# Optimization experiments

Hardware: AMD Instinct MI355X
Metric: run time of the kernel (lower is better)

Reference implementation:

```python
import jax, jax.numpy as jnp
import numpy as np

N, E = 10000, 320000
F_IN, HID, C_OUT = 256, 512, 128

def setup_inputs() -> dict:
    key = jax.random.key(0)
    ks = jax.random.split(key, 8)
    x = jax.random.normal(ks[0], (N, F_IN), dtype=jnp.float32)
    edge_index = jax.random.randint(ks[1], (2, E), 0, N, dtype=jnp.int64)
    s1 = 1.0 / np.sqrt(F_IN)
    s2 = 1.0 / np.sqrt(HID)
    # PyG SAGEConv: out = lin_l(aggr_sum(x_j)) + lin_r(x_i); lin_l has bias, lin_r does not
    W1l = jax.random.uniform(ks[2], (F_IN, HID), jnp.float32, -s1, s1)
    b1 = jnp.zeros((HID,), jnp.float32)
    W1r = jax.random.uniform(ks[3], (F_IN, HID), jnp.float32, -s1, s1)
    W2l = jax.random.uniform(ks[4], (HID, C_OUT), jnp.float32, -s2, s2)
    b2 = jnp.zeros((C_OUT,), jnp.float32)
    W2r = jax.random.uniform(ks[5], (HID, C_OUT), jnp.float32, -s2, s2)
    return {"x": x, "edge_index": edge_index, "W1l": W1l, "b1": b1,
            "W1r": W1r, "W2l": W2l, "b2": b2, "W2r": W2r}

def sage_conv(x, src, dst, Wl, b, Wr):
    # gather source-node features along edges, sum into target nodes, then linear
    agg = jax.ops.segment_sum(x[src], dst, num_segments=N)  # [N, F]
    return agg @ Wl + b + x @ Wr

def reference(x, edge_index, W1l, b1, W1r, W2l, b2, W2r):
    src, dst = edge_index[0], edge_index[1]
    h = sage_conv(x, src, dst, W1l, b1, W1r)
    h = jax.nn.relu(h)
    # F.dropout with training=False is identity (eval mode reference)
    out = sage_conv(h, src, dst, W2l, b2, W2r)
    return out
```

## Files before the change

### kernel.cpp

```cpp
#include <hip/hip_runtime.h>

#define N_NODES 10000
#define F_IN 256
#define HID 512
#define C_OUT 128
#define NEDGE 320000
#define BUCKET 128

typedef __attribute__((ext_vector_type(8))) short short8;
typedef __attribute__((ext_vector_type(4))) float floatx4;

__device__ inline float bf2f_lo(unsigned u) { union { float f; unsigned i; } v; v.i = u << 16; return v.f; }
__device__ inline float bf2f_hi(unsigned u) { union { float f; unsigned i; } v; v.i = u & 0xFFFF0000u; return v.f; }
__device__ inline unsigned short f2bf(float f) {
    union { float f; unsigned i; } v; v.f = f;
    unsigned r = (v.i + 0x7FFFu + ((v.i >> 16) & 1u)) >> 16;
    return (unsigned short)r;
}
__device__ inline void add8(float* a, uint4 v) {
    a[0] += bf2f_lo(v.x); a[1] += bf2f_hi(v.x);
    a[2] += bf2f_lo(v.y); a[3] += bf2f_hi(v.y);
    a[4] += bf2f_lo(v.z); a[5] += bf2f_hi(v.z);
    a[6] += bf2f_lo(v.w); a[7] += bf2f_hi(v.w);
}

__global__ __launch_bounds__(256)
void prep_kernel(const float4* __restrict__ xin, uint2* __restrict__ xb,
                 const float* __restrict__ W1l, const float* __restrict__ W1r,
                 const float* __restrict__ W2l, const float* __restrict__ W2r,
                 unsigned short* __restrict__ W1T, unsigned short* __restrict__ W2T,
                 int4* __restrict__ cursor4) {
    const int b = blockIdx.x;
    const int tid = threadIdx.x;
    if (b < 2500) {
        int i = b * 256 + tid;
        float4 v = xin[i];
        uint2 o;
        o.x = (unsigned)f2bf(v.x) | ((unsigned)f2bf(v.y) << 16);
        o.y = (unsigned)f2bf(v.z) | ((unsigned)f2bf(v.w) << 16);
        xb[i] = o;
        return;
    }
    if (b < 2884) {
        __shared__ float T[32][33];
        const int r = tid >> 3;
        const int c4 = (tid & 7) * 4;
        if (b < 2756) {
            int t = b - 2500;
            int kt = (t & 15) * 32, nt = (t >> 4) * 32;
            int kg = kt + r;
            const float* srcp = (kg < 256) ? (W1l + kg * 512) : (W1r + (kg - 256) * 512);
            float4 v = *(const float4*)(srcp + nt + c4);
            T[c4 + 0][r] = v.x; T[c4 + 1][r] = v.y; T[c4 + 2][r] = v.z; T[c4 + 3][r] = v.w;
            __syncthreads();
            ushort4 o;
            o.x = f2bf(T[r][c4 + 0]); o.y = f2bf(T[r][c4 + 1]);
            o.z = f2bf(T[r][c4 + 2]); o.w = f2bf(T[r][c4 + 3]);
            *(ushort4*)(W1T + (long long)(nt + r) * 512 + kt + c4) = o;
        } else {
            int t = b - 2756;
            int kt = (t & 15) * 32, col0 = (t >> 4) * 32;
            const float* Wsrc; int coloff;
            if (col0 < 128) { Wsrc = W2l; coloff = col0; } else { Wsrc = W2r; coloff = col0 - 128; }
            float4 v = *(const float4*)(Wsrc + (long long)(kt + r) * 128 + coloff + c4);
            T[c4 + 0][r] = v.x; T[c4 + 1][r] = v.y; T[c4 + 2][r] = v.z; T[c4 + 3][r] = v.w;
            __syncthreads();
            ushort4 o;
            o.x = f2bf(T[r][c4 + 0]); o.y = f2bf(T[r][c4 + 1]);
            o.z = f2bf(T[r][c4 + 2]); o.w = f2bf(T[r][c4 + 3]);
            *(ushort4*)(W2T + (long long)(col0 + r) * 512 + kt + c4) = o;
        }
        return;
    }
    {
        int i = (b - 2884) * 256 + tid;
        if (i < (N_NODES + 3) / 4) cursor4[i] = make_int4(0, 0, 0, 0);
    }
}

__global__ __launch_bounds__(256)
void fill_kernel(const int* __restrict__ src, const int* __restrict__ dst,
                 int* __restrict__ cursor, int* __restrict__ bucket, int E) {
    int e = blockIdx.x * 256 + threadIdx.x;
    if (e < E) {
        int d = dst[e];
        int pos = atomicAdd(&cursor[d], 1);
        bucket[(d << 7) + pos] = src[e];
    }
}

__global__ __launch_bounds__(256)
void gather_agg_256(const unsigned short* __restrict__ feat,
                    const int* __restrict__ cursor,
                    const int* __restrict__ bucket,
                    unsigned short* __restrict__ outp, int nnodes) {
    const int wid = (blockIdx.x * 256 + threadIdx.x) >> 6;
    if (wid >= nnodes) return;
    const int lane = threadIdx.x & 63;
    const int half = lane >> 5;
    const int sub = lane & 31;
    const long long myoff = (long long)sub * 8;
    const int cnt = __builtin_amdgcn_readfirstlane(cursor[wid]);
    const int* row = bucket + (wid << 7);

    float acc[8] = {0.f, 0.f, 0.f, 0.f, 0.f, 0.f, 0.f, 0.f};
    float accB[8] = {0.f, 0.f, 0.f, 0.f, 0.f, 0.f, 0.f, 0.f};

    int j = 0;
    for (; j + 8 <= cnt; j += 8) {
        const int4 ia = *(const int4*)(row + j);
        const int4 ib = *(const int4*)(row + j + 4);
        int i0 = half ? ia.y : ia.x;
        int i1 = half ? ia.w : ia.z;
        int i2 = half ? ib.y : ib.x;
        int i3 = half ? ib.w : ib.z;
        uint4 v0 = *(const uint4*)(feat + (long long)i0 * 256 + myoff);
        uint4 v1 = *(const uint4*)(feat + (long long)i1 * 256 + myoff);
        uint4 v2 = *(const uint4*)(feat + (long long)i2 * 256 + myoff);
        uint4 v3 = *(const uint4*)(feat + (long long)i3 * 256 + myoff);
        add8(acc, v0); add8(accB, v1); add8(acc, v2); add8(accB, v3);
    }
    for (; j + 2 <= cnt; j += 2) {
        const int2 e = *(const int2*)(row + j);
        int i0 = half ? e.y : e.x;
        uint4 v = *(const uint4*)(feat + (long long)i0 * 256 + myoff);
        add8(acc, v);
    }
    if (j < cnt) {
        int i0 = row[j];
        uint4 v = *(const uint4*)(feat + (long long)i0 * 256 + myoff);
        if (half == 0) add8(acc, v);
    }
#pragma unroll
    for (int k = 0; k < 8; ++k) acc[k] += accB[k];
#pragma unroll
    for (int k = 0; k < 8; ++k) acc[k] += __shfl_xor(acc[k], 32, 64);

    if (half == 0) {
        uint4 o;
        o.x = (unsigned)f2bf(acc[0]) | ((unsigned)f2bf(acc[1]) << 16);
        o.y = (unsigned)f2bf(acc[2]) | ((unsigned)f2bf(acc[3]) << 16);
        o.z = (unsigned)f2bf(acc[4]) | ((unsigned)f2bf(acc[5]) << 16);
        o.w = (unsigned)f2bf(acc[6]) | ((unsigned)f2bf(acc[7]) << 16);
        *(uint4*)(outp + (long long)wid * 256 + myoff) = o;
    }
}

__global__ __launch_bounds__(256)
void gather_acc_128(const unsigned short* __restrict__ feat,
                    const int* __restrict__ cursor,
                    const int* __restrict__ bucket,
                    float* __restrict__ outp, int nnodes) {
    const int wid = (blockIdx.x * 256 + threadIdx.x) >> 6;
    if (wid >= nnodes) return;
    const int lane = threadIdx.x & 63;
    const int g = lane >> 4;
    const int sub = lane & 15;
    const long long myoff = (long long)sub * 8;
    const int cnt = __builtin_amdgcn_readfirstlane(cursor[wid]);
    const int* row = bucket + (wid << 7);

    float4 c0 = make_float4(0.f, 0.f, 0.f, 0.f), c1 = c0;
    float* orow = outp + (long long)wid * 128 + sub * 8;
    if (lane < 16) {
        c0 = *(const float4*)(orow);
        c1 = *(const float4*)(orow + 4);
    }

    float acc[8] = {0.f, 0.f, 0.f, 0.f, 0.f, 0.f, 0.f, 0.f};
    float accB[8] = {0.f, 0.f, 0.f, 0.f, 0.f, 0.f, 0.f, 0.f};

    int j = 0;
    for (; j + 8 <= cnt; j += 8) {
        const int4 ia = *(const int4*)(row + j);
        const int4 ib = *(const int4*)(row + j + 4);
        int i0 = (g < 2) ? (g == 0 ? ia.x : ia.y) : (g == 2 ? ia.z : ia.w);
        int i1 = (g < 2) ? (g == 0 ? ib.x : ib.y) : (g == 2 ? ib.z : ib.w);
        uint4 v0 = *(const uint4*)(feat + (long long)i0 * 128 + myoff);
        uint4 v1 = *(const uint4*)(feat + (long long)i1 * 128 + myoff);
        add8(acc, v0); add8(accB, v1);
    }
    for (; j + 4 <= cnt; j += 4) {
        const int4 ia = *(const int4*)(row + j);
        int i0 = (g < 2) ? (g == 0 ? ia.x : ia.y) : (g == 2 ? ia.z : ia.w);
        uint4 v = *(const uint4*)(feat + (long long)i0 * 128 + myoff);
        add8(acc, v);
    }
    int rem = cnt - j;
    if (rem > 0) {
        int idx = row[j + (g < rem ? g : 0)];
        uint4 v = *(const uint4*)(feat + (long long)idx * 128 + myoff);
        if (g < rem) add8(acc, v);
    }
#pragma unroll
    for (int k = 0; k < 8; ++k) acc[k] += accB[k];
#pragma unroll
    for (int k = 0; k < 8; ++k) acc[k] += __shfl_xor(acc[k], 16, 64);
#pragma unroll
    for (int k = 0; k < 8; ++k) acc[k] += __shfl_xor(acc[k], 32, 64);

    if (lane < 16) {
        c0.x += acc[0]; c0.y += acc[1]; c0.z += acc[2]; c0.w += acc[3];
        c1.x += acc[4]; c1.y += acc[5]; c1.z += acc[6]; c1.w += acc[7];
        *(float4*)(orow) = c0;
        *(float4*)(orow + 4) = c1;
    }
}

template <int MODE>
__global__ __launch_bounds__(256)
void mfma_gemm(const unsigned short* __restrict__ A1, int K1,
               const unsigned short* __restrict__ A2, int K2,
               const unsigned short* __restrict__ BT,
               const float* __restrict__ bias,
               void* __restrict__ C0v, void* __restrict__ C1v,
               int M, int Nfull) {
    __shared__ unsigned short A_lds[64][72];
    __shared__ unsigned short B_lds[64][72];

    const int t = threadIdx.x;
    const int lane = t & 63;
    const int w = t >> 6;
    const int wm = w >> 1, wn = w & 1;
    const int l15 = lane & 15;
    const int quad = lane >> 4;
    const int row0 = blockIdx.x * 64;
    const int col0 = blockIdx.y * 64;
    const int Ktot = K1 + K2;

    floatx4 acc00 = {0.f, 0.f, 0.f, 0.f}, acc01 = acc00, acc10 = acc00, acc11 = acc00;

    for (int k0 = 0; k0 < Ktot; k0 += 64) {
        const unsigned short* Ap;
        int astride, acol;
        if (k0 < K1) { Ap = A1; astride = K1; acol = k0; }
        else         { Ap = A2; astride = K2; acol = k0 - K1; }
#pragma unroll
        for (int it = 0; it < 2; ++it) {
            int ch = t + it * 256;
            int row = ch >> 3, c16 = ch & 7;
            int gr = row0 + row; if (gr >= M) gr = M - 1;
            int4 av = *(const int4*)(Ap + (long long)gr * astride + acol + c16 * 8);
            *(int4*)&A_lds[row][c16 * 8] = av;
            int4 bv = *(const int4*)(BT + (long long)(col0 + row) * Ktot + k0 + c16 * 8);
            *(int4*)&B_lds[row][c16 * 8] = bv;
        }
        __syncthreads();
#pragma unroll
        for (int kc = 0; kc < 2; ++kc) {
            short8 a0 = *(short8*)&A_lds[wm * 32 + l15][kc * 32 + quad * 8];
            short8 a1 = *(short8*)&A_lds[wm * 32 + 16 + l15][kc * 32 + quad * 8];
            short8 b0 = *(short8*)&B_lds[wn * 32 + l15][kc * 32 + quad * 8];
            short8 b1 = *(short8*)&B_lds[wn * 32 + 16 + l15][kc * 32 + quad * 8];
            acc00 = __builtin_amdgcn_mfma_f32_16x16x32_bf16(a0, b0, acc00, 0, 0, 0);
            acc01 = __builtin_amdgcn_mfma_f32_16x16x32_bf16(a0, b1, acc01, 0, 0, 0);
            acc10 = __builtin_amdgcn_mfma_f32_16x16x32_bf16(a1, b0, acc10, 0, 0, 0);
            acc11 = __builtin_amdgcn_mfma_f32_16x16x32_bf16(a1, b1, acc11, 0, 0, 0);
        }
        __syncthreads();
    }

    const int cj0 = col0 + wn * 32 + l15;
    const int cj1 = cj0 + 16;
    const int rbase = row0 + wm * 32 + quad * 4;

    if (MODE == 0) {
        unsigned short* C0 = (unsigned short*)C0v;
        const float bi0 = bias[cj0], bi1 = bias[cj1];
        const floatx4* accs[2][2] = {{&acc00, &acc01}, {&acc10, &acc11}};
#pragma unroll
        for (int i = 0; i < 2; ++i) {
#pragma unroll
            for (int reg = 0; reg < 4; ++reg) {
                int r = rbase + i * 16 + reg;
                if (r >= M) continue;
                float v0 = fmaxf((*accs[i][0])[reg] + bi0, 0.f);
                float v1 = fmaxf((*accs[i][1])[reg] + bi1, 0.f);
                C0[(long long)r * Nfull + cj0] = f2bf(v0);
                C0[(long long)r * Nfull + cj1] = f2bf(v1);
            }
        }
    } else {
        const floatx4* accs[2][2] = {{&acc00, &acc01}, {&acc10, &acc11}};
        if (cj0 < 128) {
            unsigned short* C0 = (unsigned short*)C0v;
#pragma unroll
            for (int i = 0; i < 2; ++i) {
#pragma unroll
                for (int reg = 0; reg < 4; ++reg) {
                    int r = rbase + i * 16 + reg;
                    if (r >= M) continue;
                    C0[(long long)r * 128 + cj0] = f2bf((*accs[i][0])[reg]);
                    C0[(long long)r * 128 + cj1] = f2bf((*accs[i][1])[reg]);
                }
            }
        } else {
            float* C1 = (float*)C1v;
            const int d0 = cj0 - 128, d1 = cj1 - 128;
            const float bi0 = bias[d0], bi1 = bias[d1];
#pragma unroll
            for (int i = 0; i < 2; ++i) {
#pragma unroll
                for (int reg = 0; reg < 4; ++reg) {
                    int r = rbase + i * 16 + reg;
                    if (r >= M) continue;
                    C1[(long long)r * 128 + d0] = (*accs[i][0])[reg] + bi0;
                    C1[(long long)r * 128 + d1] = (*accs[i][1])[reg] + bi1;
                }
            }
        }
    }
}

extern "C" void kernel_launch(void* const* d_in, const int* in_sizes, int n_in,
                              void* d_out, int out_size, void* d_ws, size_t ws_size,
                              hipStream_t stream) {
    const float* x   = (const float*)d_in[0];
    const int*   ei  = (const int*)d_in[1];
    const float* W1l = (const float*)d_in[2];
    const float* b1  = (const float*)d_in[3];
    const float* W1r = (const float*)d_in[4];
    const float* W2l = (const float*)d_in[5];
    const float* b2  = (const float*)d_in[6];
    const float* W2r = (const float*)d_in[7];
    float* out = (float*)d_out;

    const int E = in_sizes[1] / 2;
    const int* src = ei;
    const int* dst = ei + E;

    char* w = (char*)d_ws;
    int* cursor  = (int*)w;             w += 10016 * sizeof(int);
    int* bucket  = (int*)w;             w += (long long)N_NODES * BUCKET * sizeof(int);
    unsigned short* xb    = (unsigned short*)w; w += (long long)N_NODES * F_IN * 2;
    unsigned short* agg1b = (unsigned short*)w; w += (long long)N_NODES * F_IN * 2;
    unsigned short* W1T   = (unsigned short*)w; w += 512 * 512 * 2;
    unsigned short* W2T   = (unsigned short*)w; w += 256 * 512 * 2;
    unsigned short* h     = (unsigned short*)w; w += (long long)N_NODES * HID * 2;
    unsigned short* p     = (unsigned short*)w; w += (long long)N_NODES * C_OUT * 2;

    prep_kernel<<<2894, 256, 0, stream>>>((const float4*)x, (uint2*)xb,
                                          W1l, W1r, W2l, W2r, W1T, W2T, (int4*)cursor);
    fill_kernel<<<(E + 255) / 256, 256, 0, stream>>>(src, dst, cursor, bucket, E);

    const int agg_blocks = (N_NODES * 64 + 255) / 256;

    gather_agg_256<<<agg_blocks, 256, 0, stream>>>(xb, cursor, bucket, agg1b, N_NODES);
    {
        dim3 grid((N_NODES + 63) / 64, HID / 64);
        mfma_gemm<0><<<grid, 256, 0, stream>>>(agg1b, F_IN, xb, F_IN, W1T, b1,
                                               (void*)h, (void*)nullptr, N_NODES, HID);
    }

    {
        dim3 grid((N_NODES + 63) / 64, 256 / 64);
        mfma_gemm<1><<<grid, 256, 0, stream>>>(h, HID, h, 0, W2T, b2,
                                               (void*)p, (void*)out, N_NODES, 256);
    }
    gather_acc_128<<<agg_blocks, 256, 0, stream>>>(p, cursor, bucket, out, N_NODES);
}
```

Measured before the change: 161.9 us.

## Enlarge GEMM tile to 128 rows and deepen unroll of gather loops

Each GEMM block now covers 128x64 outputs instead of 64x64. Each wave computes a 32x64 strip with 8 MFMA accumulators and reuses B fragments across two A fragments, which halves the number of B tile loads per output and raises MFMA work per LDS sync. Both gather kernels gain a 16-edge unrolled loop so more independent feature loads are in flight per wave. The cost is more registers and fewer blocks in the GEMM grid, which may reduce occupancy and load balance across CUs.

```diff
diff --git a/kernel.cpp b/kernel.cpp
--- a/kernel.cpp
+++ b/kernel.cpp
@@ -22,6 +22,9 @@
     a[2] += bf2f_lo(v.y); a[3] += bf2f_hi(v.y);
     a[4] += bf2f_lo(v.z); a[5] += bf2f_hi(v.z);
     a[6] += bf2f_lo(v.w); a[7] += bf2f_hi(v.w);
+}
+__device__ inline int sel4(int4 v, int g) {
+    return g == 0 ? v.x : (g == 1 ? v.y : (g == 2 ? v.z : v.w));
 }
 
 __global__ __launch_bounds__(256)
@@ -107,6 +110,30 @@
     float accB[8] = {0.f, 0.f, 0.f, 0.f, 0.f, 0.f, 0.f, 0.f};
 
     int j = 0;
+    for (; j + 16 <= cnt; j += 16) {
+        const int4 ia = *(const int4*)(row + j);
+        const int4 ib = *(const int4*)(row + j + 4);
+        const int4 ic = *(const int4*)(row + j + 8);
+        const int4 id = *(const int4*)(row + j + 12);
+        int i0 = half ? ia.y : ia.x;
+        int i1 = half ? ia.w : ia.z;
+        int i2 = half ? ib.y : ib.x;
+        int i3 = half ? ib.w : ib.z;
+        int i4 = half ? ic.y : ic.x;
+        int i5 = half ? ic.w : ic.z;
+        int i6 = half ? id.y : id.x;
+        int i7 = half ? id.w : id.z;
+        uint4 v0 = *(const uint4*)(feat + (long long)i0 * 256 + myoff);
+        uint4 v1 = *(const uint4*)(feat + (long long)i1 * 256 + myoff);
+        uint4 v2 = *(const uint4*)(feat + (long long)i2 * 256 + myoff);
+        uint4 v3 = *(const uint4*)(feat + (long long)i3 * 256 + myoff);
+        uint4 v4 = *(const uint4*)(feat + (long long)i4 * 256 + myoff);
+        uint4 v5 = *(const uint4*)(feat + (long long)i5 * 256 + myoff);
+        uint4 v6 = *(const uint4*)(feat + (long long)i6 * 256 + myoff);
+        uint4 v7 = *(const uint4*)(feat + (long long)i7 * 256 + myoff);
+        add8(acc, v0); add8(accB, v1); add8(acc, v2); add8(accB, v3);
+        add8(acc, v4); add8(accB, v5); add8(acc, v6); add8(accB, v7);
+    }
     for (; j + 8 <= cnt; j += 8) {
         const int4 ia = *(const int4*)(row + j);
         const int4 ib = *(const int4*)(row + j + 4);
@@ -171,18 +198,29 @@
     float accB[8] = {0.f, 0.f, 0.f, 0.f, 0.f, 0.f, 0.f, 0.f};
 
     int j = 0;
+    for (; j + 16 <= cnt; j += 16) {
+        const int4 ia = *(const int4*)(row + j);
+        const int4 ib = *(const int4*)(row + j + 4);
+        const int4 ic = *(const int4*)(row + j + 8);
+        const int4 id = *(const int4*)(row + j + 12);
+        int i0 = sel4(ia, g), i1 = sel4(ib, g), i2 = sel4(ic, g), i3 = sel4(id, g);
+        uint4 v0 = *(const uint4*)(feat + (long long)i0 * 128 + myoff);
+        uint4 v1 = *(const uint4*)(feat + (long long)i1 * 128 + myoff);
+        uint4 v2 = *(const uint4*)(feat + (long long)i2 * 128 + myoff);
+        uint4 v3 = *(const uint4*)(feat + (long long)i3 * 128 + myoff);
+        add8(acc, v0); add8(accB, v1); add8(acc, v2); add8(accB, v3);
+    }
     for (; j + 8 <= cnt; j += 8) {
         const int4 ia = *(const int4*)(row + j);
         const int4 ib = *(const int4*)(row + j + 4);
-        int i0 = (g < 2) ? (g == 0 ? ia.x : ia.y) : (g == 2 ? ia.z : ia.w);
-        int i1 = (g < 2) ? (g == 0 ? ib.x : ib.y) : (g == 2 ? ib.z : ib.w);
+        int i0 = sel4(ia, g), i1 = sel4(ib, g);
         uint4 v0 = *(const uint4*)(feat + (long long)i0 * 128 + myoff);
         uint4 v1 = *(const uint4*)(feat + (long long)i1 * 128 + myoff);
         add8(acc, v0); add8(accB, v1);
     }
     for (; j + 4 <= cnt; j += 4) {
         const int4 ia = *(const int4*)(row + j);
-        int i0 = (g < 2) ? (g == 0 ? ia.x : ia.y) : (g == 2 ? ia.z : ia.w);
+        int i0 = sel4(ia, g);
         uint4 v = *(const uint4*)(feat + (long long)i0 * 128 + myoff);
         add8(acc, v);
     }
@@ -215,20 +253,26 @@
                const float* __restrict__ bias,
                void* __restrict__ C0v, void* __restrict__ C1v,
                int M, int Nfull) {
-    __shared__ unsigned short A_lds[64][72];
+    __shared__ unsigned short A_lds[128][72];
     __shared__ unsigned short B_lds[64][72];
 
     const int t = threadIdx.x;
     const int lane = t & 63;
     const int w = t >> 6;
-    const int wm = w >> 1, wn = w & 1;
     const int l15 = lane & 15;
     const int quad = lane >> 4;
-    const int row0 = blockIdx.x * 64;
+    const int row0 = blockIdx.x * 128;
     const int col0 = blockIdx.y * 64;
     const int Ktot = K1 + K2;
 
-    floatx4 acc00 = {0.f, 0.f, 0.f, 0.f}, acc01 = acc00, acc10 = acc00, acc11 = acc00;
+    floatx4 acc[2][4];
+#pragma unroll
+    for (int i = 0; i < 2; ++i)
+#pragma unroll
+        for (int cf = 0; cf < 4; ++cf) acc[i][cf] = (floatx4){0.f, 0.f, 0.f, 0.f};
+
+    const int srow = t >> 3;
+    const int scol = (t & 7) * 8;
 
     for (int k0 = 0; k0 < Ktot; k0 += 64) {
         const unsigned short* Ap;
@@ -236,76 +280,82 @@
         if (k0 < K1) { Ap = A1; astride = K1; acol = k0; }
         else         { Ap = A2; astride = K2; acol = k0 - K1; }
 #pragma unroll
+        for (int it = 0; it < 4; ++it) {
+            int row = srow + it * 32;
+            int gr = row0 + row; if (gr >= M) gr = M - 1;
+            *(int4*)&A_lds[row][scol] = *(const int4*)(Ap + (long long)gr * astride + acol + scol);
+        }
+#pragma unroll
         for (int it = 0; it < 2; ++it) {
-            int ch = t + it * 256;
-            int row = ch >> 3, c16 = ch & 7;
-            int gr = row0 + row; if (gr >= M) gr = M - 1;
-            int4 av = *(const int4*)(Ap + (long long)gr * astride + acol + c16 * 8);
-            *(int4*)&A_lds[row][c16 * 8] = av;
-            int4 bv = *(const int4*)(BT + (long long)(col0 + row) * Ktot + k0 + c16 * 8);
-            *(int4*)&B_lds[row][c16 * 8] = bv;
+            int row = srow + it * 32;
+            *(int4*)&B_lds[row][scol] = *(const int4*)(BT + (long long)(col0 + row) * Ktot + k0 + scol);
         }
         __syncthreads();
 #pragma unroll
         for (int kc = 0; kc < 2; ++kc) {
-            short8 a0 = *(short8*)&A_lds[wm * 32 + l15][kc * 32 + quad * 8];
-            short8 a1 = *(short8*)&A_lds[wm * 32 + 16 + l15][kc * 32 + quad * 8];
-            short8 b0 = *(short8*)&B_lds[wn * 32 + l15][kc * 32 + quad * 8];
-            short8 b1 = *(short8*)&B_lds[wn * 32 + 16 + l15][kc * 32 + quad * 8];
-            acc00 = __builtin_amdgcn_mfma_f32_16x16x32_bf16(a0, b0, acc00, 0, 0, 0);
-            acc01 = __builtin_amdgcn_mfma_f32_16x16x32_bf16(a0, b1, acc01, 0, 0, 0);
-            acc10 = __builtin_amdgcn_mfma_f32_16x16x32_bf16(a1, b0, acc10, 0, 0, 0);
-            acc11 = __builtin_amdgcn_mfma_f32_16x16x32_bf16(a1, b1, acc11, 0, 0, 0);
+            short8 a0 = *(short8*)&A_lds[w * 32 + l15][kc * 32 + quad * 8];
+            short8 a1 = *(short8*)&A_lds[w * 32 + 16 + l15][kc * 32 + quad * 8];
+            short8 bb[4];
+#pragma unroll
+            for (int cf = 0; cf < 4; ++cf)
+                bb[cf] = *(short8*)&B_lds[cf * 16 + l15][kc * 32 + quad * 8];
+#pragma unroll
+            for (int cf = 0; cf < 4; ++cf) {
+                acc[0][cf] = __builtin_amdgcn_mfma_f32_16x16x32_bf16(a0, bb[cf], acc[0][cf], 0, 0, 0);
+                acc[1][cf] = __builtin_amdgcn_mfma_f32_16x16x32_bf16(a1, bb[cf], acc[1][cf], 0, 0, 0);
+            }
         }
         __syncthreads();
     }
 
-    const int cj0 = col0 + wn * 32 + l15;
-    const int cj1 = cj0 + 16;
-    const int rbase = row0 + wm * 32 + quad * 4;
+    const int rbase = row0 + w * 32 + quad * 4;
 
     if (MODE == 0) {
         unsigned short* C0 = (unsigned short*)C0v;
-        const float bi0 = bias[cj0], bi1 = bias[cj1];
-        const floatx4* accs[2][2] = {{&acc00, &acc01}, {&acc10, &acc11}};
-#pragma unroll
-        for (int i = 0; i < 2; ++i) {
-#pragma unroll
-            for (int reg = 0; reg < 4; ++reg) {
-                int r = rbase + i * 16 + reg;
-                if (r >= M) continue;
-                float v0 = fmaxf((*accs[i][0])[reg] + bi0, 0.f);
-                float v1 = fmaxf((*accs[i][1])[reg] + bi1, 0.f);
-                C0[(long long)r * Nfull + cj0] = f2bf(v0);
-                C0[(long long)r * Nfull + cj1] = f2bf(v1);
-            }
-        }
-    } else {
-        const floatx4* accs[2][2] = {{&acc00, &acc01}, {&acc10, &acc11}};
-        if (cj0 < 128) {
-            unsigned short* C0 = (unsigned short*)C0v;
+#pragma unroll
+        for (int cf = 0; cf < 4; ++cf) {
+            const int cj = col0 + cf * 16 + l15;
+            const float bi = bias[cj];
 #pragma unroll
             for (int i = 0; i < 2; ++i) {
 #pragma unroll
                 for (int reg = 0; reg < 4; ++reg) {
                     int r = rbase + i * 16 + reg;
                     if (r >= M) continue;
-                    C0[(long long)r * 128 + cj0] = f2bf((*accs[i][0])[reg]);
-                    C0[(long long)r * 128 + cj1] = f2bf((*accs[i][1])[reg]);
+                    C0[(long long)r * Nfull + cj] = f2bf(fmaxf(acc[i][cf][reg] + bi, 0.f));
+                }
+            }
+        }
+    } else {
+        if (col0 < 128) {
+            unsigned short* C0 = (unsigned short*)C0v;
+#pragma unroll
+            for (int cf = 0; cf < 4; ++cf) {
+                const int cj = col0 + cf * 16 + l15;
+#pragma unroll
+                for (int i = 0; i < 2; ++i) {
+#pragma unroll
+                    for (int reg = 0; reg < 4; ++reg) {
+                        int r = rbase + i * 16 + reg;
+                        if (r >= M) continue;
+                        C0[(long long)r * 128 + cj] = f2bf(acc[i][cf][reg]);
+                    }
                 }
             }
         } else {
             float* C1 = (float*)C1v;
-            const int d0 = cj0 - 128, d1 = cj1 - 128;
-            const float bi0 = bias[d0], bi1 = bias[d1];
-#pragma unroll
-            for (int i = 0; i < 2; ++i) {
-#pragma unroll
-                for (int reg = 0; reg < 4; ++reg) {
-                    int r = rbase + i * 16 + reg;
-                    if (r >= M) continue;
-                    C1[(long long)r * 128 + d0] = (*accs[i][0])[reg] + bi0;
-                    C1[(long long)r * 128 + d1] = (*accs[i][1])[reg] + bi1;
+#pragma unroll
+            for (int cf = 0; cf < 4; ++cf) {
+                const int d = col0 - 128 + cf * 16 + l15;
+                const float bi = bias[d];
+#pragma unroll
+                for (int i = 0; i < 2; ++i) {
+#pragma unroll
+                    for (int reg = 0; reg < 4; ++reg) {
+                        int r = rbase + i * 16 + reg;
+                        if (r >= M) continue;
+                        C1[(long long)r * 128 + d] = acc[i][cf][reg] + bi;
+                    }
                 }
             }
         }
@@ -347,13 +397,13 @@
 
     gather_agg_256<<<agg_blocks, 256, 0, stream>>>(xb, cursor, bucket, agg1b, N_NODES);
     {
-        dim3 grid((N_NODES + 63) / 64, HID / 64);
+        dim3 grid((N_NODES + 127) / 128, HID / 64);
         mfma_gemm<0><<<grid, 256, 0, stream>>>(agg1b, F_IN, xb, F_IN, W1T, b1,
                                                (void*)h, (void*)nullptr, N_NODES, HID);
     }
 
     {
-        dim3 grid((N_NODES + 63) / 64, 256 / 64);
+        dim3 grid((N_NODES + 127) / 128, 256 / 64);
         mfma_gemm<1><<<grid, 256, 0, stream>>>(h, HID, h, 0, W2T, b2,
                                                (void*)p, (void*)out, N_NODES, 256);
     }
```

After: 161.5 us. No clear change (-0.2%).

## Fuse all stages into one cooperative persistent kernel with grid syncs

Applied to the files above, without the earlier changes.

Replaces the six separate launches (prep, fill, gather, two GEMMs, gather) with a single cooperative kernel of 512 persistent blocks. The stages are separated by grid.sync and use grid-stride loops, with GEMM tiles distributed round-robin. This removes inter-kernel launch gaps. In exchange, occupancy is capped at 512 blocks, the grid barriers add cost, and load balance inside each stage may get worse. The gather loops are also unrolled to 16 edges per iteration to keep more loads in flight.

```diff
diff --git a/kernel.cpp b/kernel.cpp
--- a/kernel.cpp
+++ b/kernel.cpp
@@ -1,11 +1,14 @@
 #include <hip/hip_runtime.h>
+#include <hip/hip_cooperative_groups.h>
+
+namespace cg = cooperative_groups;
 
 #define N_NODES 10000
 #define F_IN 256
 #define HID 512
 #define C_OUT 128
-#define NEDGE 320000
 #define BUCKET 128
+#define GRID_BLOCKS 512
 
 typedef __attribute__((ext_vector_type(8))) short short8;
 typedef __attribute__((ext_vector_type(4))) float floatx4;
@@ -23,82 +26,118 @@
     a[4] += bf2f_lo(v.z); a[5] += bf2f_hi(v.z);
     a[6] += bf2f_lo(v.w); a[7] += bf2f_hi(v.w);
 }
-
-__global__ __launch_bounds__(256)
-void prep_kernel(const float4* __restrict__ xin, uint2* __restrict__ xb,
-                 const float* __restrict__ W1l, const float* __restrict__ W1r,
-                 const float* __restrict__ W2l, const float* __restrict__ W2r,
-                 unsigned short* __restrict__ W1T, unsigned short* __restrict__ W2T,
-                 int4* __restrict__ cursor4) {
-    const int b = blockIdx.x;
-    const int tid = threadIdx.x;
-    if (b < 2500) {
-        int i = b * 256 + tid;
-        float4 v = xin[i];
-        uint2 o;
-        o.x = (unsigned)f2bf(v.x) | ((unsigned)f2bf(v.y) << 16);
-        o.y = (unsigned)f2bf(v.z) | ((unsigned)f2bf(v.w) << 16);
-        xb[i] = o;
-        return;
-    }
-    if (b < 2884) {
-        __shared__ float T[32][33];
-        const int r = tid >> 3;
-        const int c4 = (tid & 7) * 4;
-        if (b < 2756) {
-            int t = b - 2500;
-            int kt = (t & 15) * 32, nt = (t >> 4) * 32;
-            int kg = kt + r;
-            const float* srcp = (kg < 256) ? (W1l + kg * 512) : (W1r + (kg - 256) * 512);
-            float4 v = *(const float4*)(srcp + nt + c4);
-            T[c4 + 0][r] = v.x; T[c4 + 1][r] = v.y; T[c4 + 2][r] = v.z; T[c4 + 3][r] = v.w;
+__device__ inline int sel4(int4 v, int g) {
+    return g == 0 ? v.x : (g == 1 ? v.y : (g == 2 ? v.z : v.w));
+}
+
+template <int MODE>
+__device__ void gemm_stage(char* smem,
+                           const unsigned short* __restrict__ A1, int K1,
+                           const unsigned short* __restrict__ A2, int K2,
+                           const unsigned short* __restrict__ BT,
+                           const float* __restrict__ bias,
+                           unsigned short* __restrict__ C0, float* __restrict__ C1,
+                           int M, int Nfull, int ntilesM, int ntilesN) {
+    unsigned short (*A_lds)[72] = (unsigned short(*)[72])smem;
+    unsigned short (*B_lds)[72] = (unsigned short(*)[72])(smem + 64 * 72 * 2);
+
+    const int t = threadIdx.x;
+    const int lane = t & 63;
+    const int w = t >> 6;
+    const int wm = w >> 1, wn = w & 1;
+    const int l15 = lane & 15;
+    const int quad = lane >> 4;
+    const int Ktot = K1 + K2;
+    const int ntiles = ntilesM * ntilesN;
+
+    const int srow = t >> 3;
+    const int scol = (t & 7) * 8;
+
+    for (int tile = blockIdx.x; tile < ntiles; tile += gridDim.x) {
+        const int row0 = (tile / ntilesN) * 64;
+        const int col0 = (tile % ntilesN) * 64;
+
+        floatx4 acc00 = {0.f, 0.f, 0.f, 0.f}, acc01 = acc00, acc10 = acc00, acc11 = acc00;
+
+        for (int k0 = 0; k0 < Ktot; k0 += 64) {
+            const unsigned short* Ap;
+            int astride, acol;
+            if (k0 < K1) { Ap = A1; astride = K1; acol = k0; }
+            else         { Ap = A2; astride = K2; acol = k0 - K1; }
+#pragma unroll
+            for (int it = 0; it < 2; ++it) {
+                int row = srow + it * 32;
+                int gr = row0 + row; if (gr >= M) gr = M - 1;
+                *(int4*)&A_lds[row][scol] = *(const int4*)(Ap + (long long)gr * astride + acol + scol);
+                *(int4*)&B_lds[row][scol] = *(const int4*)(BT + (long long)(col0 + row) * Ktot + k0 + scol);
+            }
             __syncthreads();
-            ushort4 o;
-            o.x = f2bf(T[r][c4 + 0]); o.y = f2bf(T[r][c4 + 1]);
-            o.z = f2bf(T[r][c4 + 2]); o.w = f2bf(T[r][c4 + 3]);
-            *(ushort4*)(W1T + (long long)(nt + r) * 512 + kt + c4) = o;
+#pragma unroll
+            for (int kc = 0; kc < 2; ++kc) {
+                short8 a0 = *(short8*)&A_lds[wm * 32 + l15][kc * 32 + quad * 8];
+                short8 a1 = *(short8*)&A_lds[wm * 32 + 16 + l15][kc * 32 + quad * 8];
+                short8 b0 = *(short8*)&B_lds[wn * 32 + l15][kc * 32 + quad * 8];
+                short8 b1 = *(short8*)&B_lds[wn * 32 + 16 + l15][kc * 32 + quad * 8];
+                acc00 = __builtin_amdgcn_mfma_f32_16x16x32_bf16(a0, b0, acc00, 0, 0, 0);
+                acc01 = __builtin_amdgcn_mfma_f32_16x16x32_bf16(a0, b1, acc01, 0, 0, 0);
+                acc10 = __builtin_amdgcn_mfma_f32_16x16x32_bf16(a1, b0, acc10, 0, 0, 0);
+                acc11 = __builtin_amdgcn_mfma_f32_16x16x32_bf16(a1, b1, acc11, 0, 0, 0);
+            }
+            __syncthreads();
+        }
+
+        const int cj0 = col0 + wn * 32 + l15;
+        const int cj1 = cj0 + 16;
+        const int rbase = row0 + wm * 32 + quad * 4;
+        const floatx4* accs[2][2] = {{&acc00, &acc01}, {&acc10, &acc11}};
+
+        if (MODE == 0) {
+            const float bi0 = bias[cj0], bi1 = bias[cj1];
+#pragma unroll
+            for (int i = 0; i < 2; ++i) {
+#pragma unroll
+                for (int reg = 0; reg < 4; ++reg) {
+                    int r = rbase + i * 16 + reg;
+                    if (r >= M) continue;
+                    C0[(long long)r * Nfull + cj0] = f2bf(fmaxf((*accs[i][0])[reg] + bi0, 0.f));
+                    C0[(long long)r * Nfull + cj1] = f2bf(fmaxf((*accs[i][1])[reg] + bi1, 0.f));
+                }
+            }
         } else {
-            int t = b - 2756;
-            int kt = (t & 15) * 32, col0 = (t >> 4) * 32;
-            const float* Wsrc; int coloff;
-            if (col0 < 128) { Wsrc = W2l; coloff = col0; } else { Wsrc = W2r; coloff = col0 - 128; }
-            float4 v = *(const float4*)(Wsrc + (long long)(kt + r) * 128 + coloff + c4);
-            T[c4 + 0][r] = v.x; T[c4 + 1][r] = v.y; T[c4 + 2][r] = v.z; T[c4 + 3][r] = v.w;
-            __syncthreads();
-            ushort4 o;
-            o.x = f2bf(T[r][c4 + 0]); o.y = f2bf(T[r][c4 + 1]);
-            o.z = f2bf(T[r][c4 + 2]); o.w = f2bf(T[r][c4 + 3]);
-            *(ushort4*)(W2T + (long long)(col0 + r) * 512 + kt + c4) = o;
+            if (cj0 < 128) {
+#pragma unroll
+                for (int i = 0; i < 2; ++i) {
+#pragma unroll
+                    for (int reg = 0; reg < 4; ++reg) {
+                        int r = rbase + i * 16 + reg;
+                        if (r >= M) continue;
+                        C0[(long long)r * 128 + cj0] = f2bf((*accs[i][0])[reg]);
+                        C0[(long long)r * 128 + cj1] = f2bf((*accs[i][1])[reg]);
+                    }
+                }
+            } else {
+                const int d0 = cj0 - 128, d1 = cj1 - 128;
+                const float bi0 = bias[d0], bi1 = bias[d1];
+#pragma unroll
+                for (int i = 0; i < 2; ++i) {
+#pragma unroll
+                    for (int reg = 0; reg < 4; ++reg) {
+                        int r = rbase + i * 16 + reg;
+                        if (r >= M) continue;
+                        C1[(long long)r * 128 + d0] = (*accs[i][0])[reg] + bi0;
+                        C1[(long long)r * 128 + d1] = (*accs[i][1])[reg] + bi1;
+                    }
+                }
+            }
         }
-        return;
-    }
-    {
-        int i = (b - 2884) * 256 + tid;
-        if (i < (N_NODES + 3) / 4) cursor4[i] = make_int4(0, 0, 0, 0);
-    }
-}
-
-__global__ __launch_bounds__(256)
-void fill_kernel(const int* __restrict__ src, const int* __restrict__ dst,
-                 int* __restrict__ cursor, int* __restrict__ bucket, int E) {
-    int e = blockIdx.x * 256 + threadIdx.x;
-    if (e < E) {
-        int d = dst[e];
-        int pos = atomicAdd(&cursor[d], 1);
-        bucket[(d << 7) + pos] = src[e];
-    }
-}
-
-__global__ __launch_bounds__(256)
-void gather_agg_256(const unsigned short* __restrict__ feat,
-                    const int* __restrict__ cursor,
-                    const int* __restrict__ bucket,
-                    unsigned short* __restrict__ outp, int nnodes) {
-    const int wid = (blockIdx.x * 256 + threadIdx.x) >> 6;
-    if (wid >= nnodes) return;
-    const int lane = threadIdx.x & 63;
-    const int half = lane >> 5;
-    const int sub = lane & 31;
+    }
+}
+
+__device__ void gather1_node(const unsigned short* __restrict__ feat,
+                             const int* __restrict__ cursor,
+                             const int* __restrict__ bucket,
+                             unsigned short* __restrict__ outp, int wid,
+                             int half, int sub) {
     const long long myoff = (long long)sub * 8;
     const int cnt = __builtin_amdgcn_readfirstlane(cursor[wid]);
     const int* row = bucket + (wid << 7);
@@ -107,6 +146,30 @@
     float accB[8] = {0.f, 0.f, 0.f, 0.f, 0.f, 0.f, 0.f, 0.f};
 
     int j = 0;
+    for (; j + 16 <= cnt; j += 16) {
+        const int4 ia = *(const int4*)(row + j);
+        const int4 ib = *(const int4*)(row + j + 4);
+        const int4 ic = *(const int4*)(row + j + 8);
+        const int4 id = *(const int4*)(row + j + 12);
+        int i0 = half ? ia.y : ia.x;
+        int i1 = half ? ia.w : ia.z;
+        int i2 = half ? ib.y : ib.x;
+        int i3 = half ? ib.w : ib.z;
+        int i4 = half ? ic.y : ic.x;
+        int i5 = half ? ic.w : ic.z;
+        int i6 = half ? id.y : id.x;
+        int i7 = half ? id.w : id.z;
+        uint4 v0 = *(const uint4*)(feat + (long long)i0 * 256 + myoff);
+        uint4 v1 = *(const uint4*)(feat + (long long)i1 * 256 + myoff);
+        uint4 v2 = *(const uint4*)(feat + (long long)i2 * 256 + myoff);
+        uint4 v3 = *(const uint4*)(feat + (long long)i3 * 256 + myoff);
+        uint4 v4 = *(const uint4*)(feat + (long long)i4 * 256 + myoff);
+        uint4 v5 = *(const uint4*)(feat + (long long)i5 * 256 + myoff);
+        uint4 v6 = *(const uint4*)(feat + (long long)i6 * 256 + myoff);
+        uint4 v7 = *(const uint4*)(feat + (long long)i7 * 256 + myoff);
+        add8(acc, v0); add8(accB, v1); add8(acc, v2); add8(accB, v3);
+        add8(acc, v4); add8(accB, v5); add8(acc, v6); add8(accB, v7);
+    }
     for (; j + 8 <= cnt; j += 8) {
         const int4 ia = *(const int4*)(row + j);
         const int4 ib = *(const int4*)(row + j + 4);
@@ -146,16 +209,11 @@
     }
 }
 
-__global__ __launch_bounds__(256)
-void gather_acc_128(const unsigned short* __restrict__ feat,
-                    const int* __restrict__ cursor,
-                    const int* __restrict__ bucket,
-                    float* __restrict__ outp, int nnodes) {
-    const int wid = (blockIdx.x * 256 + threadIdx.x) >> 6;
-    if (wid >= nnodes) return;
-    const int lane = threadIdx.x & 63;
-    const int g = lane >> 4;
-    const int sub = lane & 15;
+__device__ void gather2_node(const unsigned short* __restrict__ feat,
+                             const int* __restrict__ cursor,
+                             const int* __restrict__ bucket,
+                             float* __restrict__ outp, int wid,
+                             int g, int sub, int lane) {
     const long long myoff = (long long)sub * 8;
     const int cnt = __builtin_amdgcn_readfirstlane(cursor[wid]);
     const int* row = bucket + (wid << 7);
@@ -171,18 +229,29 @@
     float accB[8] = {0.f, 0.f, 0.f, 0.f, 0.f, 0.f, 0.f, 0.f};
 
     int j = 0;
+    for (; j + 16 <= cnt; j += 16) {
+        const int4 ia = *(const int4*)(row + j);
+        const int4 ib = *(const int4*)(row + j + 4);
+        const int4 ic = *(const int4*)(row + j + 8);
+        const int4 id = *(const int4*)(row + j + 12);
+        int i0 = sel4(ia, g), i1 = sel4(ib, g), i2 = sel4(ic, g), i3 = sel4(id, g);
+        uint4 v0 = *(const uint4*)(feat + (long long)i0 * 128 + myoff);
+        uint4 v1 = *(const uint4*)(feat + (long long)i1 * 128 + myoff);
+        uint4 v2 = *(const uint4*)(feat + (long long)i2 * 128 + myoff);
+        uint4 v3 = *(const uint4*)(feat + (long long)i3 * 128 + myoff);
+        add8(acc, v0); add8(accB, v1); add8(acc, v2); add8(accB, v3);
+    }
     for (; j + 8 <= cnt; j += 8) {
         const int4 ia = *(const int4*)(row + j);
         const int4 ib = *(const int4*)(row + j + 4);
-        int i0 = (g < 2) ? (g == 0 ? ia.x : ia.y) : (g == 2 ? ia.z : ia.w);
-        int i1 = (g < 2) ? (g == 0 ? ib.x : ib.y) : (g == 2 ? ib.z : ib.w);
+        int i0 = sel4(ia, g), i1 = sel4(ib, g);
         uint4 v0 = *(const uint4*)(feat + (long long)i0 * 128 + myoff);
         uint4 v1 = *(const uint4*)(feat + (long long)i1 * 128 + myoff);
         add8(acc, v0); add8(accB, v1);
     }
     for (; j + 4 <= cnt; j += 4) {
         const int4 ia = *(const int4*)(row + j);
-        int i0 = (g < 2) ? (g == 0 ? ia.x : ia.y) : (g == 2 ? ia.z : ia.w);
+        int i0 = sel4(ia, g);
         uint4 v = *(const uint4*)(feat + (long long)i0 * 128 + myoff);
         add8(acc, v);
     }
@@ -207,108 +276,104 @@
     }
 }
 
-template <int MODE>
-__global__ __launch_bounds__(256)
-void mfma_gemm(const unsigned short* __restrict__ A1, int K1,
-               const unsigned short* __restrict__ A2, int K2,
-               const unsigned short* __restrict__ BT,
-               const float* __restrict__ bias,
-               void* __restrict__ C0v, void* __restrict__ C1v,
-               int M, int Nfull) {
-    __shared__ unsigned short A_lds[64][72];
-    __shared__ unsigned short B_lds[64][72];
-
-    const int t = threadIdx.x;
-    const int lane = t & 63;
-    const int w = t >> 6;
-    const int wm = w >> 1, wn = w & 1;
-    const int l15 = lane & 15;
-    const int quad = lane >> 4;
-    const int row0 = blockIdx.x * 64;
-    const int col0 = blockIdx.y * 64;
-    const int Ktot = K1 + K2;
-
-    floatx4 acc00 = {0.f, 0.f, 0.f, 0.f}, acc01 = acc00, acc10 = acc00, acc11 = acc00;
-
-    for (int k0 = 0; k0 < Ktot; k0 += 64) {
-        const unsigned short* Ap;
-        int astride, acol;
-        if (k0 < K1) { Ap = A1; astride = K1; acol = k0; }
-        else         { Ap = A2; astride = K2; acol = k0 - K1; }
-#pragma unroll
-        for (int it = 0; it < 2; ++it) {
-            int ch = t + it * 256;
-            int row = ch >> 3, c16 = ch & 7;
-            int gr = row0 + row; if (gr >= M) gr = M - 1;
-            int4 av = *(const int4*)(Ap + (long long)gr * astride + acol + c16 * 8);
-            *(int4*)&A_lds[row][c16 * 8] = av;
-            int4 bv = *(const int4*)(BT + (long long)(col0 + row) * Ktot + k0 + c16 * 8);
-            *(int4*)&B_lds[row][c16 * 8] = bv;
+__global__ __launch_bounds__(256, 2)
+void mega_kernel(const float4* __restrict__ xin,
+                 const int* __restrict__ src, const int* __restrict__ dst,
+                 const float* __restrict__ W1l, const float* __restrict__ b1,
+                 const float* __restrict__ W1r,
+                 const float* __restrict__ W2l, const float* __restrict__ b2,
+                 const float* __restrict__ W2r,
+                 float* __restrict__ out,
+                 unsigned short* __restrict__ xb,
+                 unsigned short* __restrict__ agg1b,
+                 unsigned short* __restrict__ W1T,
+                 unsigned short* __restrict__ W2T,
+                 unsigned short* __restrict__ h,
+                 unsigned short* __restrict__ p,
+                 int* __restrict__ cursor, int* __restrict__ bucket, int E) {
+    cg::grid_group grid = cg::this_grid();
+    __shared__ __align__(16) char smem[64 * 72 * 2 * 2];
+
+    const int tid = threadIdx.x;
+    const int bid = blockIdx.x;
+    const int gthread = bid * 256 + tid;
+    const int nthreads = gridDim.x * 256;
+    const int lane = tid & 63;
+    const int wid0 = gthread >> 6;
+    const int nwaves = nthreads >> 6;
+
+    for (int i = gthread; i < N_NODES * F_IN / 4; i += nthreads) {
+        float4 v = xin[i];
+        uint2 o;
+        o.x = (unsigned)f2bf(v.x) | ((unsigned)f2bf(v.y) << 16);
+        o.y = (unsigned)f2bf(v.z) | ((unsigned)f2bf(v.w) << 16);
+        ((uint2*)xb)[i] = o;
+    }
+    if (bid < 384) {
+        float (*T)[33] = (float(*)[33])smem;
+        const int r = tid >> 3;
+        const int c4 = (tid & 7) * 4;
+        if (bid < 256) {
+            int kt = (bid & 15) * 32, nt = (bid >> 4) * 32;
+            int kg = kt + r;
+            const float* srcp = (kg < 256) ? (W1l + kg * 512) : (W1r + (kg - 256) * 512);
+            float4 v = *(const float4*)(srcp + nt + c4);
+            T[c4 + 0][r] = v.x; T[c4 + 1][r] = v.y; T[c4 + 2][r] = v.z; T[c4 + 3][r] = v.w;
+            __syncthreads();
+            ushort4 o;
+            o.x = f2bf(T[r][c4 + 0]); o.y = f2bf(T[r][c4 + 1]);
+            o.z = f2bf(T[r][c4 + 2]); o.w = f2bf(T[r][c4 + 3]);
+            *(ushort4*)(W1T + (long long)(nt + r) * 512 + kt + c4) = o;
+        } else {
+            int t2 = bid - 256;
+            int kt = (t2 & 15) * 32, col0 = (t2 >> 4) * 32;
+            const float* Wsrc; int coloff;
+            if (col0 < 128) { Wsrc = W2l; coloff = col0; } else { Wsrc = W2r; coloff = col0 - 128; }
+            float4 v = *(const float4*)(Wsrc + (long long)(kt + r) * 128 + coloff + c4);
+            T[c4 + 0][r] = v.x; T[c4 + 1][r] = v.y; T[c4 + 2][r] = v.z; T[c4 + 3][r] = v.w;
+            __syncthreads();
+            ushort4 o;
+            o.x = f2bf(T[r][c4 + 0]); o.y = f2bf(T[r][c4 + 1]);
+            o.z = f2bf(T[r][c4 + 2]); o.w = f2bf(T[r][c4 + 3]);
+            *(ushort4*)(W2T + (long long)(col0 + r) * 512 + kt + c4) = o;
         }
-        __syncthreads();
-#pragma unroll
-        for (int kc = 0; kc < 2; ++kc) {
-            short8 a0 = *(short8*)&A_lds[wm * 32 + l15][kc * 32 + quad * 8];
-            short8 a1 = *(short8*)&A_lds[wm * 32 + 16 + l15][kc * 32 + quad * 8];
-            short8 b0 = *(short8*)&B_lds[wn * 32 + l15][kc * 32 + quad * 8];
-            short8 b1 = *(short8*)&B_lds[wn * 32 + 16 + l15][kc * 32 + quad * 8];
-            acc00 = __builtin_amdgcn_mfma_f32_16x16x32_bf16(a0, b0, acc00, 0, 0, 0);
-            acc01 = __builtin_amdgcn_mfma_f32_16x16x32_bf16(a0, b1, acc01, 0, 0, 0);
-            acc10 = __builtin_amdgcn_mfma_f32_16x16x32_bf16(a1, b0, acc10, 0, 0, 0);
-            acc11 = __builtin_amdgcn_mfma_f32_16x16x32_bf16(a1, b1, acc11, 0, 0, 0);
-        }
-        __syncthreads();
-    }
-
-    const int cj0 = col0 + wn * 32 + l15;
-    const int cj1 = cj0 + 16;
-    const int rbase = row0 + wm * 32 + quad * 4;
-
-    if (MODE == 0) {
-        unsigned short* C0 = (unsigned short*)C0v;
-        const float bi0 = bias[cj0], bi1 = bias[cj1];
-        const floatx4* accs[2][2] = {{&acc00, &acc01}, {&acc10, &acc11}};
-#pragma unroll
-        for (int i = 0; i < 2; ++i) {
-#pragma unroll
-            for (int reg = 0; reg < 4; ++reg) {
-                int r = rbase + i * 16 + reg;
-                if (r >= M) continue;
-                float v0 = fmaxf((*accs[i][0])[reg] + bi0, 0.f);
-                float v1 = fmaxf((*accs[i][1])[reg] + bi1, 0.f);
-                C0[(long long)r * Nfull + cj0] = f2bf(v0);
-                C0[(long long)r * Nfull + cj1] = f2bf(v1);
-            }
-        }
-    } else {
-        const floatx4* accs[2][2] = {{&acc00, &acc01}, {&acc10, &acc11}};
-        if (cj0 < 128) {
-            unsigned short* C0 = (unsigned short*)C0v;
-#pragma unroll
-            for (int i = 0; i < 2; ++i) {
-#pragma unroll
-                for (int reg = 0; reg < 4; ++reg) {
-                    int r = rbase + i * 16 + reg;
-                    if (r >= M) continue;
-                    C0[(long long)r * 128 + cj0] = f2bf((*accs[i][0])[reg]);
-                    C0[(long long)r * 128 + cj1] = f2bf((*accs[i][1])[reg]);
-                }
-            }
-        } else {
-            float* C1 = (float*)C1v;
-            const int d0 = cj0 - 128, d1 = cj1 - 128;
-            const float bi0 = bias[d0], bi1 = bias[d1];
-#pragma unroll
-            for (int i = 0; i < 2; ++i) {
-#pragma unroll
-                for (int reg = 0; reg < 4; ++reg) {
-                    int r = rbase + i * 16 + reg;
-                    if (r >= M) continue;
-                    C1[(long long)r * 128 + d0] = (*accs[i][0])[reg] + bi0;
-                    C1[(long long)r * 128 + d1] = (*accs[i][1])[reg] + bi1;
-                }
-            }
-        }
+    }
+    if (gthread < (N_NODES + 3) / 4) ((int4*)cursor)[gthread] = make_int4(0, 0, 0, 0);
+
+    grid.sync();
+
+    for (int e = gthread; e < E; e += nthreads) {
+        int d = dst[e];
+        int pos = atomicAdd(&cursor[d], 1);
+        bucket[(d << 7) + pos] = src[e];
+    }
+
+    grid.sync();
+
+    {
+        const int half = lane >> 5;
+        const int sub = lane & 31;
+        for (int n = wid0; n < N_NODES; n += nwaves)
+            gather1_node(xb, cursor, bucket, agg1b, n, half, sub);
+    }
+
+    grid.sync();
+
+    gemm_stage<0>(smem, agg1b, F_IN, xb, F_IN, W1T, b1, h, nullptr,
+                  N_NODES, HID, (N_NODES + 63) / 64, HID / 64);
+
+    grid.sync();
+
+    gemm_stage<1>(smem, h, HID, h, 0, W2T, b2, p, out,
+                  N_NODES, 256, (N_NODES + 63) / 64, 256 / 64);
+
+    grid.sync();
+
+    {
+        const int g = lane >> 4;
+        const int sub = lane & 15;
+        for (int n = wid0; n < N_NODES; n += nwaves)
+            gather2_node(p, cursor, bucket, out, n, g, sub, lane);
     }
 }
 
@@ -325,7 +390,7 @@
     const float* W2r = (const float*)d_in[7];
     float* out = (float*)d_out;
 
-    const int E = in_sizes[1] / 2;
+    int E = in_sizes[1] / 2;
     const int* src = ei;
     const int* dst = ei + E;
 
@@ -339,23 +404,16 @@
     unsigned short* h     = (unsigned short*)w; w += (long long)N_NODES * HID * 2;
     unsigned short* p     = (unsigned short*)w; w += (long long)N_NODES * C_OUT * 2;
 
-    prep_kernel<<<2894, 256, 0, stream>>>((const float4*)x, (uint2*)xb,
-                                          W1l, W1r, W2l, W2r, W1T, W2T, (int4*)cursor);
-    fill_kernel<<<(E + 255) / 256, 256, 0, stream>>>(src, dst, cursor, bucket, E);
-
-    const int agg_blocks = (N_NODES * 64 + 255) / 256;
-
-    gather_agg_256<<<agg_blocks, 256, 0, stream>>>(xb, cursor, bucket, agg1b, N_NODES);
-    {
-        dim3 grid((N_NODES + 63) / 64, HID / 64);
-        mfma_gemm<0><<<grid, 256, 0, stream>>>(agg1b, F_IN, xb, F_IN, W1T, b1,
-                                               (void*)h, (void*)nullptr, N_NODES, HID);
-    }
-
-    {
-        dim3 grid((N_NODES + 63) / 64, 256 / 64);
-        mfma_gemm<1><<<grid, 256, 0, stream>>>(h, HID, h, 0, W2T, b2,
-                                               (void*)p, (void*)out, N_NODES, 256);
-    }
-    gather_acc_128<<<agg_blocks, 256, 0, stream>>>(p, cursor, bucket, out, N_NODES);
-}
+    const float4* xin = (const float4*)x;
+    void* args[] = {
+        (void*)&xin, (void*)&src, (void*)&dst,
+        (void*)&W1l, (void*)&b1, (void*)&W1r,
+        (void*)&W2l, (void*)&b2, (void*)&W2r,
+        (void*)&out,
+        (void*)&xb, (void*)&agg1b, (void*)&W1T, (void*)&W2T,
+        (void*)&h, (void*)&p,
+        (void*)&cursor, (void*)&bucket, (void*)&E
+    };
+    hipLaunchCooperativeKernel((void*)mega_kernel, dim3(GRID_BLOCKS), dim3(256),
+                               args, 0, stream);
+}
```

Result: slower. 485.2 us (+199.6%).
